# Kernel optimization log

Measured on AMD Instinct MI355X. Metric: run time of the kernel, lower is better.

## Reference

```python
import jax, jax.numpy as jnp
import numpy as np

N = 100_000          # nodes
E = 1_600_000        # edges (avg degree 16)
NODE_SCA, NODE_VEC = 4, 3
EDGE_SCA, EDGE_VEC = 6, 3
OUT_SCA, OUT_VEC = 16, 16
CUTOFF = 10.0
EPS = 1e-6
SLOPE_VN = 0.2       # VNLeakyReLU negative slope (SurfGen default)
SLOPE_SCA = 0.01     # nn.LeakyReLU default


def setup_inputs() -> dict:
    key = jax.random.key(0)
    ks = jax.random.split(key, 22)
    rn = lambda k, s: jax.random.normal(k, s, dtype=jnp.float32)
    return {
        # forward args
        'node_sca': rn(ks[0], (N, NODE_SCA)),
        'node_vec': rn(ks[1], (N, NODE_VEC, 3)),
        'edge_sca': rn(ks[2], (E, EDGE_SCA)),
        'edge_vec': rn(ks[3], (E, EDGE_VEC, 3)),
        'gds_dist': jax.random.uniform(ks[4], (E,), dtype=jnp.float32) * 12.0,
        'edge_index': jax.random.randint(ks[5], (2, E), 0, N),
        # message projections (Linear weights stored [in,out])
        'W_nss': rn(ks[6], (NODE_SCA, OUT_SCA)) * 0.3, 'b_nss': rn(ks[7], (OUT_SCA,)) * 0.1,
        'W_ess': rn(ks[8], (EDGE_SCA, OUT_SCA)) * 0.3, 'b_ess': rn(ks[9], (OUT_SCA,)) * 0.1,
        'W_nsv': rn(ks[10], (NODE_SCA, OUT_SCA)) * 0.3, 'b_nsv': rn(ks[11], (OUT_SCA,)) * 0.1,
        'W_esv': rn(ks[12], (EDGE_SCA, OUT_SCA)) * 0.3, 'b_esv': rn(ks[13], (OUT_SCA,)) * 0.1,
        'W_nvv': rn(ks[14], (NODE_VEC, OUT_VEC)) * 0.3,   # VNLinear (no bias)
        'W_evv': rn(ks[15], (EDGE_VEC, OUT_VEC)) * 0.3,
        # GVPerceptronVN(16,16,16,16): GVLinear (dim_hid = 16) + VN LeakyReLU
        'W_lv':  rn(ks[16], (OUT_VEC, OUT_VEC)) * 0.25,   # lin_vector   (no bias)
        'W_lv2': rn(ks[17], (OUT_VEC, OUT_VEC)) * 0.25,   # lin_vector2  (no bias)
        'W_ls':  rn(ks[18], (OUT_VEC + OUT_SCA, OUT_SCA)) * 0.25,  # lin_scalar (no bias)
        'W_gate': rn(ks[19], (OUT_SCA, OUT_VEC)) * 0.25, 'b_gate': rn(ks[20], (OUT_VEC,)) * 0.1,
        'W_dir': rn(ks[21], (OUT_VEC, OUT_VEC)) * 0.25,   # VNLeakyReLU direction (no bias)
    }


def vn_linear(x, W):
    # x: [n, c_in, 3], W: [c_in, c_out] -> [n, c_out, 3]
    return jnp.einsum('nci,co->noi', x, W)


def reference(node_sca, node_vec, edge_sca, edge_vec, gds_dist, edge_index,
              W_nss, b_nss, W_ess, b_ess, W_nsv, b_nsv, W_esv, b_esv,
              W_nvv, W_evv, W_lv, W_lv2, W_ls, W_gate, b_gate, W_dir):
    src = edge_index[0]
    num_nodes = node_sca.shape[0]

    # cosine cutoff coefficient
    coeff = 0.5 * (jnp.cos(gds_dist * (jnp.pi / CUTOFF)) + 1.0)
    coeff = coeff * (gds_dist <= CUTOFF) * (gds_dist >= 0.0)  # [E]

    # scalar message: gather node proj, mix with edge proj, cutoff-weight
    node_ss = node_sca @ W_nss + b_nss                          # [N,16]
    edge_ss = edge_sca @ W_ess + b_ess                          # [E,16]
    msg_sca = node_ss[src] * edge_ss * coeff[:, None]           # [E,16]

    # vector message
    node_vv = vn_linear(node_vec, W_nvv)                        # [N,16,3]
    edge_vv = vn_linear(edge_vec, W_evv)                        # [E,16,3]
    node_sv = node_sca @ W_nsv + b_nsv                          # [N,16]
    edge_sv = edge_sca @ W_esv + b_esv                          # [E,16]
    msg_vec = (node_vv[src] * edge_sv[:, :, None]
               + node_sv[src][:, :, None] * edge_vv) * coeff[:, None, None]  # [E,16,3]

    # scatter_sum into source nodes (matches original's edge_index[0])
    aggr_sca = jax.ops.segment_sum(msg_sca, src, num_segments=num_nodes)  # [N,16]
    aggr_vec = jax.ops.segment_sum(msg_vec, src, num_segments=num_nodes)  # [N,16,3]

    # --- GVPerceptronVN: GVLinear ---
    v_inter = vn_linear(aggr_vec, W_lv)                          # [N,16,3]
    v_norm = jnp.sqrt(jnp.sum(v_inter * v_inter, axis=-1))       # [N,16]
    out_sca = jnp.concatenate([v_norm, aggr_sca], axis=-1) @ W_ls  # [N,16]
    out_vec = vn_linear(v_inter, W_lv2)                          # [N,16,3]
    gate = jax.nn.sigmoid(out_sca @ W_gate + b_gate)[:, :, None]
    out_vec = gate * out_vec

    # --- VNLeakyReLU on vectors ---
    d = vn_linear(out_vec, W_dir)                                # [N,16,3]
    dot = jnp.sum(out_vec * d, axis=-1, keepdims=True)
    mask = (dot >= 0).astype(out_vec.dtype)
    d_norm_sq = jnp.sum(d * d, axis=-1, keepdims=True)
    out_vec = SLOPE_VN * out_vec + (1.0 - SLOPE_VN) * (
        mask * out_vec + (1.0 - mask) * (out_vec - (dot / (d_norm_sq + EPS)) * d))

    # LeakyReLU on scalars
    out_sca = jnp.where(out_sca >= 0, out_sca, SLOPE_SCA * out_sca)
    return out_sca, out_vec
```

## Files before the change

kernel.cpp:

```cpp
#include <hip/hip_runtime.h>
#include <hip/hip_fp16.h>
#include <math.h>

#define CUTOFF_F 10.0f
#define PI_OVER_CUTOFF 0.31415926535897931f
#define KCAP 64


__global__ __launch_bounds__(256) void count_edges(
    const int* __restrict__ eidx,
    int* __restrict__ count,
    int* __restrict__ slotOf,
    int E)
{
    int e = blockIdx.x * blockDim.x + threadIdx.x;
    if (e >= E) return;
    int src = eidx[e];
    slotOf[e] = atomicAdd(&count[src], 1);
}

__global__ __launch_bounds__(256) void scan_block_sums(
    const int* __restrict__ count, int* __restrict__ blockSums, int N)
{
    __shared__ int sdata[256];
    int t = threadIdx.x;
    int i = blockIdx.x * 256 + t;
    sdata[t] = (i < N) ? count[i] : 0;
    __syncthreads();
    for (int off = 128; off > 0; off >>= 1) {
        if (t < off) sdata[t] += sdata[t + off];
        __syncthreads();
    }
    if (t == 0) blockSums[blockIdx.x] = sdata[0];
}

__global__ __launch_bounds__(1024) void scan_exclusive_small(
    int* __restrict__ blockSums, int M)
{
    __shared__ int s[1024];
    int t = threadIdx.x;
    int orig = (t < M) ? blockSums[t] : 0;
    s[t] = orig;
    __syncthreads();
    for (int off = 1; off < 1024; off <<= 1) {
        int v = (t >= off) ? s[t - off] : 0;
        __syncthreads();
        s[t] += v;
        __syncthreads();
    }
    if (t < M) blockSums[t] = s[t] - orig;
}

__global__ __launch_bounds__(256) void scan_final(
    const int* __restrict__ count, const int* __restrict__ blockSums,
    int* __restrict__ offsets, int N)
{
    __shared__ int s[256];
    int t = threadIdx.x;
    int i = blockIdx.x * 256 + t;
    int orig = (i < N) ? count[i] : 0;
    s[t] = orig;
    __syncthreads();
    for (int off = 1; off < 256; off <<= 1) {
        int v = (t >= off) ? s[t - off] : 0;
        __syncthreads();
        s[t] += v;
        __syncthreads();
    }
    if (i < N) offsets[i] = s[t] - orig + blockSums[blockIdx.x];
}

__global__ __launch_bounds__(256) void scatter_payload(
    const float* __restrict__ edge_sca,
    const float* __restrict__ edge_vec,
    const float* __restrict__ gds,
    const int* __restrict__ eidx,
    const int* __restrict__ slotOf,
    const int* __restrict__ offsets,
    __half* __restrict__ payload,
    int E)
{
    int e = blockIdx.x * blockDim.x + threadIdx.x;
    if (e >= E) return;

    int src = eidx[e];
    float d = gds[e];
    float c = 0.0f;
    if (d >= 0.0f && d <= CUTOFF_F)
        c = 0.5f * (__cosf(d * PI_OVER_CUTOFF) + 1.0f);

    const float* es = edge_sca + (size_t)e * 6;
    const float* ev = edge_vec + (size_t)e * 9;

    union { __half h[16]; uint4 u[2]; } pk;
#pragma unroll
    for (int i = 0; i < 6; ++i) pk.h[i] = __float2half(c * es[i]);
    pk.h[6] = __float2half(c);
#pragma unroll
    for (int i = 0; i < 9; ++i) pk.h[7 + i] = __float2half(c * ev[i]);

    uint4* pb = (uint4*)(payload + (size_t)(offsets[src] + slotOf[e]) * 16);
    pb[0] = pk.u[0];
    pb[1] = pk.u[1];
}

__global__ __launch_bounds__(256) void fill_buckets(
    const int* __restrict__ eidx, int* __restrict__ count,
    int* __restrict__ bucket, int E)
{
    int e = blockIdx.x * blockDim.x + threadIdx.x;
    if (e >= E) return;
    int src = eidx[e];
    int slot = atomicAdd(&count[src], 1);
    if (slot < KCAP) bucket[src * KCAP + slot] = e;
}

__global__ __launch_bounds__(256) void edge_aggregate(
    const float* __restrict__ edge_sca, const float* __restrict__ edge_vec,
    const float* __restrict__ gds, const int* __restrict__ eidx,
    float* __restrict__ aggr, int E)
{
    int e = blockIdx.x * blockDim.x + threadIdx.x;
    if (e >= E) return;
    int src = eidx[e];
    float d = gds[e];
    float coeff = 0.0f;
    if (d >= 0.0f && d <= CUTOFF_F)
        coeff = 0.5f * (__cosf(d * PI_OVER_CUTOFF) + 1.0f);
    float* base = aggr + (size_t)src * 16;
    const float* es = edge_sca + (size_t)e * 6;
    const float* ev = edge_vec + (size_t)e * 9;
#pragma unroll
    for (int c = 0; c < 6; ++c) atomicAdd(base + c, coeff * es[c]);
    atomicAdd(base + 6, coeff);
#pragma unroll
    for (int k = 0; k < 9; ++k) atomicAdd(base + 7 + k, coeff * ev[k]);
}

__global__ __launch_bounds__(256) void node_fused(
    const float* __restrict__ node_sca,
    const float* __restrict__ node_vec,
    const float* __restrict__ edge_sca,
    const float* __restrict__ edge_vec,
    const float* __restrict__ gds,
    const int* __restrict__ count,
    const int* __restrict__ bucket,
    const int* __restrict__ offsets,
    const __half* __restrict__ payload,
    const float* __restrict__ aggr,
    const float* __restrict__ W_nss, const float* __restrict__ b_nss,
    const float* __restrict__ W_ess, const float* __restrict__ b_ess,
    const float* __restrict__ W_nsv, const float* __restrict__ b_nsv,
    const float* __restrict__ W_esv, const float* __restrict__ b_esv,
    const float* __restrict__ W_nvv, const float* __restrict__ W_evv,
    const float* __restrict__ W_lv,  const float* __restrict__ W_lv2,
    const float* __restrict__ W_ls,
    const float* __restrict__ W_gate, const float* __restrict__ b_gate,
    const float* __restrict__ W_dir,
    float* __restrict__ out,
    int N, int mode)
{
    __shared__ float sW_nss[64],  sb_nss[16];
    __shared__ float sW_ess[96],  sb_ess[16];
    __shared__ float sW_nsv[64],  sb_nsv[16];
    __shared__ float sW_esv[96],  sb_esv[16];
    __shared__ float sW_nvv[48],  sW_evv[48];
    __shared__ float sW_lv[256],  sW_lv2[256];
    __shared__ float sW_ls[512];
    __shared__ float sW_gate[256], sb_gate[16];
    __shared__ float sW_dir[256];

    __shared__ float s_in  [16 * 33];
    __shared__ float s_avec[16 * 49];
    __shared__ float s_cat [16 * 33];
    __shared__ float s_vint[16 * 49];
    __shared__ float s_osca[16 * 17];
    __shared__ float s_ovec[16 * 49];

    const int t = threadIdx.x;
    {
        for (int i = t; i < 64;  i += 256) { sW_nss[i] = W_nss[i]; sW_nsv[i] = W_nsv[i]; }
        for (int i = t; i < 96;  i += 256) { sW_ess[i] = W_ess[i]; sW_esv[i] = W_esv[i]; }
        for (int i = t; i < 48;  i += 256) { sW_nvv[i] = W_nvv[i]; sW_evv[i] = W_evv[i]; }
        for (int i = t; i < 256; i += 256) {
            sW_lv[i]   = W_lv[i];
            sW_lv2[i]  = W_lv2[i];
            sW_gate[i] = W_gate[i];
            sW_dir[i]  = W_dir[i];
        }
        for (int i = t; i < 512; i += 256) sW_ls[i] = W_ls[i];
        if (t < 16) {
            sb_nss[t]  = b_nss[t];
            sb_ess[t]  = b_ess[t];
            sb_nsv[t]  = b_nsv[t];
            sb_esv[t]  = b_esv[t];
            sb_gate[t] = b_gate[t];
        }
    }

    const int slot = t >> 4;
    const int o    = t & 15;
    const int n    = blockIdx.x * 16 + slot;
    const bool valid = (n < N);

    if (valid) {
        if (o < 4) s_in[slot * 33 + o]     = node_sca[(size_t)n * 4 + o];
        if (o < 9) s_in[slot * 33 + 4 + o] = node_vec[(size_t)n * 9 + o];
    }

    if (mode == 2) {
        float a0 = 0.f, a1 = 0.f, a2 = 0.f, a3 = 0.f;
        if (valid) {
            int cnt = count[n];
            const __half* p = payload + (size_t)offsets[n] * 16 + o;
            int s = 0;
            for (; s + 3 < cnt; s += 4) {
                a0 += __half2float(p[(size_t)(s + 0) * 16]);
                a1 += __half2float(p[(size_t)(s + 1) * 16]);
                a2 += __half2float(p[(size_t)(s + 2) * 16]);
                a3 += __half2float(p[(size_t)(s + 3) * 16]);
            }
            for (; s < cnt; ++s)
                a0 += __half2float(p[(size_t)s * 16]);
            s_in[slot * 33 + 13 + o] = (a0 + a1) + (a2 + a3);
        }
    } else if (mode == 1) {
        float acc = 0.0f;
        int cnt = valid ? count[n] : 0;
        if (cnt > KCAP) cnt = KCAP;
        const int* bk = bucket + (size_t)n * KCAP;
        for (int s = 0; s < cnt; ++s) {
            int e = bk[s];
            float d = gds[e];
            float coeff = 0.0f;
            if (d >= 0.0f && d <= CUTOFF_F)
                coeff = 0.5f * (__cosf(d * PI_OVER_CUTOFF) + 1.0f);
            float feat;
            if (o < 6)       feat = edge_sca[(size_t)e * 6 + o];
            else if (o == 6) feat = 1.0f;
            else             feat = edge_vec[(size_t)e * 9 + (o - 7)];
            acc += coeff * feat;
        }
        if (valid) s_in[slot * 33 + 13 + o] = acc;
    } else {
        if (valid) s_in[slot * 33 + 13 + o] = aggr[(size_t)n * 16 + o];
    }
    __syncthreads();

    const float* in = s_in + slot * 33;

    float nss = sb_nss[o], nsv = sb_nsv[o];
#pragma unroll
    for (int c = 0; c < 4; ++c) {
        float x = in[c];
        nss += x * sW_nss[c * 16 + o];
        nsv += x * sW_nsv[c * 16 + o];
    }
    float nvv0 = 0.f, nvv1 = 0.f, nvv2 = 0.f;
#pragma unroll
    for (int c = 0; c < 3; ++c) {
        float w = sW_nvv[c * 16 + o];
        nvv0 += in[4 + c * 3 + 0] * w;
        nvv1 += in[4 + c * 3 + 1] * w;
        nvv2 += in[4 + c * 3 + 2] * w;
    }
    float cc = in[19];
    float es = cc * sb_ess[o], ev = cc * sb_esv[o];
#pragma unroll
    for (int c = 0; c < 6; ++c) {
        float a = in[13 + c];
        es += a * sW_ess[c * 16 + o];
        ev += a * sW_esv[c * 16 + o];
    }
    float EV0 = 0.f, EV1 = 0.f, EV2 = 0.f;
#pragma unroll
    for (int c = 0; c < 3; ++c) {
        float w = sW_evv[c * 16 + o];
        EV0 += in[20 + c * 3 + 0] * w;
        EV1 += in[20 + c * 3 + 1] * w;
        EV2 += in[20 + c * 3 + 2] * w;
    }

    float asca = nss * es;
    float av0 = nvv0 * ev + nsv * EV0;
    float av1 = nvv1 * ev + nsv * EV1;
    float av2 = nvv2 * ev + nsv * EV2;
    s_avec[slot * 49 + o * 3 + 0] = av0;
    s_avec[slot * 49 + o * 3 + 1] = av1;
    s_avec[slot * 49 + o * 3 + 2] = av2;
    s_cat[slot * 33 + 16 + o] = asca;
    __syncthreads();

    float vi0 = 0.f, vi1 = 0.f, vi2 = 0.f;
#pragma unroll
    for (int c = 0; c < 16; ++c) {
        float w = sW_lv[c * 16 + o];
        const float* a = &s_avec[slot * 49 + c * 3];
        vi0 += a[0] * w; vi1 += a[1] * w; vi2 += a[2] * w;
    }
    float vnorm = sqrtf(vi0 * vi0 + vi1 * vi1 + vi2 * vi2);
    s_vint[slot * 49 + o * 3 + 0] = vi0;
    s_vint[slot * 49 + o * 3 + 1] = vi1;
    s_vint[slot * 49 + o * 3 + 2] = vi2;
    s_cat[slot * 33 + o] = vnorm;
    __syncthreads();

    float osca = 0.f;
#pragma unroll
    for (int c = 0; c < 32; ++c)
        osca += s_cat[slot * 33 + c] * sW_ls[c * 16 + o];
    float ov0 = 0.f, ov1 = 0.f, ov2 = 0.f;
#pragma unroll
    for (int c = 0; c < 16; ++c) {
        float w = sW_lv2[c * 16 + o];
        const float* a = &s_vint[slot * 49 + c * 3];
        ov0 += a[0] * w; ov1 += a[1] * w; ov2 += a[2] * w;
    }
    s_osca[slot * 17 + o] = osca;
    __syncthreads();

    float g = sb_gate[o];
#pragma unroll
    for (int c = 0; c < 16; ++c)
        g += s_osca[slot * 17 + c] * sW_gate[c * 16 + o];
    g = 1.0f / (1.0f + __expf(-g));
    ov0 *= g; ov1 *= g; ov2 *= g;
    s_ovec[slot * 49 + o * 3 + 0] = ov0;
    s_ovec[slot * 49 + o * 3 + 1] = ov1;
    s_ovec[slot * 49 + o * 3 + 2] = ov2;
    __syncthreads();

    float dv0 = 0.f, dv1 = 0.f, dv2 = 0.f;
#pragma unroll
    for (int c = 0; c < 16; ++c) {
        float w = sW_dir[c * 16 + o];
        const float* a = &s_ovec[slot * 49 + c * 3];
        dv0 += a[0] * w; dv1 += a[1] * w; dv2 += a[2] * w;
    }
    float dot = ov0 * dv0 + ov1 * dv1 + ov2 * dv2;
    if (dot < 0.0f) {
        float dn = dv0 * dv0 + dv1 * dv1 + dv2 * dv2;
        float f = 0.8f * dot / (dn + 1e-6f);
        ov0 -= f * dv0; ov1 -= f * dv1; ov2 -= f * dv2;
    }

    if (valid) {
        float so = (osca >= 0.0f) ? osca : 0.01f * osca;
        out[(size_t)n * 16 + o] = so;
        size_t vb = (size_t)N * 16 + (size_t)n * 48 + (size_t)o * 3;
        out[vb + 0] = ov0;
        out[vb + 1] = ov1;
        out[vb + 2] = ov2;
    }
}

extern "C" void kernel_launch(void* const* d_in, const int* in_sizes, int n_in,
                              void* d_out, int out_size, void* d_ws, size_t ws_size,
                              hipStream_t stream)
{
    const float* node_sca = (const float*)d_in[0];
    const float* node_vec = (const float*)d_in[1];
    const float* edge_sca = (const float*)d_in[2];
    const float* edge_vec = (const float*)d_in[3];
    const float* gds      = (const float*)d_in[4];
    const int*   eidx     = (const int*)d_in[5];

    const int N = in_sizes[0] / 4;
    const int E = in_sizes[4];

    int*    count     = (int*)d_ws;
    int*    offsets   = count + N;
    int*    blockSums = offsets + N;
    int*    slotOf    = blockSums + 1024;
    size_t  hdr_bytes = ((size_t)(2 * N + 1024 + E) * 4 + 63) & ~(size_t)63;
    __half* payload   = (__half*)((char*)d_ws + hdr_bytes);
    size_t  need_csr  = hdr_bytes + (size_t)E * 16 * sizeof(__half);
    size_t  need_bkt  = (size_t)N * (1 + KCAP) * sizeof(int);

    const int nBlocksN = (N + 255) / 256;

    int mode;
    if (ws_size >= need_csr && nBlocksN <= 1024) mode = 2;
    else if (ws_size >= need_bkt)                mode = 1;
    else                                         mode = 0;

    int* bucket = count + N;
    float* aggr = (float*)d_ws;

    if (mode == 2) {
        hipMemsetAsync(count, 0, (size_t)N * sizeof(int), stream);
        count_edges<<<(E + 255) / 256, 256, 0, stream>>>(eidx, count, slotOf, E);
        scan_block_sums<<<nBlocksN, 256, 0, stream>>>(count, blockSums, N);
        scan_exclusive_small<<<1, 1024, 0, stream>>>(blockSums, nBlocksN);
        scan_final<<<nBlocksN, 256, 0, stream>>>(count, blockSums, offsets, N);
        scatter_payload<<<(E + 255) / 256, 256, 0, stream>>>(
            edge_sca, edge_vec, gds, eidx, slotOf, offsets, payload, E);
    } else if (mode == 1) {
        hipMemsetAsync(count, 0, (size_t)N * sizeof(int), stream);
        fill_buckets<<<(E + 255) / 256, 256, 0, stream>>>(eidx, count, bucket, E);
    } else {
        hipMemsetAsync(aggr, 0, (size_t)N * 16 * sizeof(float), stream);
        edge_aggregate<<<(E + 255) / 256, 256, 0, stream>>>(
            edge_sca, edge_vec, gds, eidx, aggr, E);
    }

    node_fused<<<(N + 15) / 16, 256, 0, stream>>>(
        node_sca, node_vec, edge_sca, edge_vec, gds,
        count, bucket, offsets, payload, aggr,
        (const float*)d_in[6],  (const float*)d_in[7],
        (const float*)d_in[8],  (const float*)d_in[9],
        (const float*)d_in[10], (const float*)d_in[11],
        (const float*)d_in[12], (const float*)d_in[13],
        (const float*)d_in[14], (const float*)d_in[15],
        (const float*)d_in[16], (const float*)d_in[17],
        (const float*)d_in[18],
        (const float*)d_in[19], (const float*)d_in[20],
        (const float*)d_in[21],
        (float*)d_out, N, mode);
}
```

Measured before the change: 358.0 us.

## Replace CSR build with fixed-capacity per-node buckets plus atomic overflow

Adds a new default mode that drops the count/scan/scatter CSR pipeline. A single kernel computes cutoff-scaled edge payloads and atomically claims a slot in a fixed 32-entry per-node bucket, stored as fp16. Edges beyond capacity are atomically added into an fp32 overflow array. The node kernel then sums the bucket entries plus the overflow. This cuts kernel launches and one pass over the edges, at the cost of a larger workspace, a bigger memset, and strided reads across sparsely filled buckets.

New measurement: 305.7 us. 14.6% less time.

```diff
diff --git a/kernel.cpp b/kernel.cpp
--- a/kernel.cpp
+++ b/kernel.cpp
@@ -5,13 +5,55 @@
 #define CUTOFF_F 10.0f
 #define PI_OVER_CUTOFF 0.31415926535897931f
 #define KCAP 64
-
-
-__global__ __launch_bounds__(256) void count_edges(
+#define KCAP3 32
+
+__global__ __launch_bounds__(256) void bucket_scatter(
+    const float* __restrict__ edge_sca,
+    const float* __restrict__ edge_vec,
+    const float* __restrict__ gds,
     const int* __restrict__ eidx,
     int* __restrict__ count,
-    int* __restrict__ slotOf,
+    __half* __restrict__ bucket,
+    float* __restrict__ aggr,
     int E)
+{
+    int e = blockIdx.x * blockDim.x + threadIdx.x;
+    if (e >= E) return;
+
+    int src = eidx[e];
+    float d = gds[e];
+    float c = 0.0f;
+    if (d >= 0.0f && d <= CUTOFF_F)
+        c = 0.5f * (__cosf(d * PI_OVER_CUTOFF) + 1.0f);
+
+    const float* es = edge_sca + (size_t)e * 6;
+    const float* ev = edge_vec + (size_t)e * 9;
+
+    float f[16];
+#pragma unroll
+    for (int i = 0; i < 6; ++i) f[i] = c * es[i];
+    f[6] = c;
+#pragma unroll
+    for (int i = 0; i < 9; ++i) f[7 + i] = c * ev[i];
+
+    int slot = atomicAdd(&count[src], 1);
+    if (slot < KCAP3) {
+        union { __half h[16]; uint4 u[2]; } pk;
+#pragma unroll
+        for (int i = 0; i < 16; ++i) pk.h[i] = __float2half(f[i]);
+        uint4* pb = (uint4*)(bucket + ((size_t)src * KCAP3 + slot) * 16);
+        pb[0] = pk.u[0];
+        pb[1] = pk.u[1];
+    } else {
+        float* base = aggr + (size_t)src * 16;
+#pragma unroll
+        for (int i = 0; i < 16; ++i) atomicAdd(base + i, f[i]);
+    }
+}
+
+__global__ __launch_bounds__(256) void count_edges(
+    const int* __restrict__ eidx, int* __restrict__ count,
+    int* __restrict__ slotOf, int E)
 {
     int e = blockIdx.x * blockDim.x + threadIdx.x;
     if (e >= E) return;
@@ -71,34 +113,26 @@
 }
 
 __global__ __launch_bounds__(256) void scatter_payload(
-    const float* __restrict__ edge_sca,
-    const float* __restrict__ edge_vec,
-    const float* __restrict__ gds,
-    const int* __restrict__ eidx,
-    const int* __restrict__ slotOf,
-    const int* __restrict__ offsets,
-    __half* __restrict__ payload,
-    int E)
+    const float* __restrict__ edge_sca, const float* __restrict__ edge_vec,
+    const float* __restrict__ gds, const int* __restrict__ eidx,
+    const int* __restrict__ slotOf, const int* __restrict__ offsets,
+    __half* __restrict__ payload, int E)
 {
     int e = blockIdx.x * blockDim.x + threadIdx.x;
     if (e >= E) return;
-
     int src = eidx[e];
     float d = gds[e];
     float c = 0.0f;
     if (d >= 0.0f && d <= CUTOFF_F)
         c = 0.5f * (__cosf(d * PI_OVER_CUTOFF) + 1.0f);
-
     const float* es = edge_sca + (size_t)e * 6;
     const float* ev = edge_vec + (size_t)e * 9;
-
     union { __half h[16]; uint4 u[2]; } pk;
 #pragma unroll
     for (int i = 0; i < 6; ++i) pk.h[i] = __float2half(c * es[i]);
     pk.h[6] = __float2half(c);
 #pragma unroll
     for (int i = 0; i < 9; ++i) pk.h[7 + i] = __float2half(c * ev[i]);
-
     uint4* pb = (uint4*)(payload + (size_t)(offsets[src] + slotOf[e]) * 16);
     pb[0] = pk.u[0];
     pb[1] = pk.u[1];
@@ -208,7 +242,25 @@
         if (o < 9) s_in[slot * 33 + 4 + o] = node_vec[(size_t)n * 9 + o];
     }
 
-    if (mode == 2) {
+    if (mode == 3) {
+        float a0 = 0.f, a1 = 0.f, a2 = 0.f, a3 = 0.f;
+        if (valid) {
+            int cnt = count[n];
+            if (cnt > KCAP3) cnt = KCAP3;
+            const __half* p = payload + (size_t)n * KCAP3 * 16 + o;
+            int s = 0;
+            for (; s + 3 < cnt; s += 4) {
+                a0 += __half2float(p[(s + 0) * 16]);
+                a1 += __half2float(p[(s + 1) * 16]);
+                a2 += __half2float(p[(s + 2) * 16]);
+                a3 += __half2float(p[(s + 3) * 16]);
+            }
+            for (; s < cnt; ++s)
+                a0 += __half2float(p[s * 16]);
+            a1 += aggr[(size_t)n * 16 + o];
+            s_in[slot * 33 + 13 + o] = (a0 + a1) + (a2 + a3);
+        }
+    } else if (mode == 2) {
         float a0 = 0.f, a1 = 0.f, a2 = 0.f, a3 = 0.f;
         if (valid) {
             int cnt = count[n];
@@ -368,6 +420,12 @@
     const int N = in_sizes[0] / 4;
     const int E = in_sizes[4];
 
+    int*    count3  = (int*)d_ws;
+    float*  aggr3   = (float*)(count3 + N);
+    __half* bucket3 = (__half*)(aggr3 + (size_t)N * 16);
+    size_t  need3   = (size_t)N * 4 + (size_t)N * 64
+                    + (size_t)N * KCAP3 * 16 * sizeof(__half);
+
     int*    count     = (int*)d_ws;
     int*    offsets   = count + N;
     int*    blockSums = offsets + N;
@@ -380,12 +438,33 @@
     const int nBlocksN = (N + 255) / 256;
 
     int mode;
-    if (ws_size >= need_csr && nBlocksN <= 1024) mode = 2;
-    else if (ws_size >= need_bkt)                mode = 1;
-    else                                         mode = 0;
+    if (ws_size >= need3)                          mode = 3;
+    else if (ws_size >= need_csr && nBlocksN <= 1024) mode = 2;
+    else if (ws_size >= need_bkt)                  mode = 1;
+    else                                           mode = 0;
 
     int* bucket = count + N;
     float* aggr = (float*)d_ws;
+
+    if (mode == 3) {
+        hipMemsetAsync(count3, 0, (size_t)N * 4 + (size_t)N * 64, stream);
+        bucket_scatter<<<(E + 255) / 256, 256, 0, stream>>>(
+            edge_sca, edge_vec, gds, eidx, count3, bucket3, aggr3, E);
+        node_fused<<<(N + 15) / 16, 256, 0, stream>>>(
+            node_sca, node_vec, edge_sca, edge_vec, gds,
+            count3, bucket, offsets, bucket3, aggr3,
+            (const float*)d_in[6],  (const float*)d_in[7],
+            (const float*)d_in[8],  (const float*)d_in[9],
+            (const float*)d_in[10], (const float*)d_in[11],
+            (const float*)d_in[12], (const float*)d_in[13],
+            (const float*)d_in[14], (const float*)d_in[15],
+            (const float*)d_in[16], (const float*)d_in[17],
+            (const float*)d_in[18],
+            (const float*)d_in[19], (const float*)d_in[20],
+            (const float*)d_in[21],
+            (float*)d_out, N, 3);
+        return;
+    }
 
     if (mode == 2) {
         hipMemsetAsync(count, 0, (size_t)N * sizeof(int), stream);
```
